# Kernel tuning notes

Measured on AMD Instinct MI355X. Metric: run time of the kernel, lower is better.

## Reference

```python
import jax, jax.numpy as jnp
import numpy as np

# Dimensions
B_, T_, IN_ = 8, 1024, 512          # batch, seq_len, in_dim
D_ = 1024                           # latent_dim (hidden_size)
I_ = 2048                           # intermediate_size
N_ = 64                             # state_size
H_ = 16                             # ssm_num_head
P_ = I_ // H_                       # head_dim = 128
K_ = 3                              # conv_kernel
L_ = 4                              # num_layer
OUT_, CB_ = 512, 1024               # out_dim, num_code_book
CONV_DIM = I_ + 2 * N_              # 2176
PROJ = I_ + CONV_DIM + H_           # in_proj width of mixer = 4240


def setup_inputs() -> dict:
    key = jax.random.key(0)
    ks = jax.random.split(key, 16)
    s = 0.02
    inp = {
        "x": jax.random.normal(ks[0], (B_, T_, IN_), jnp.float32),
        "in_w": jax.random.normal(ks[1], (IN_, D_), jnp.float32) * s,
        "in_b": jnp.zeros((D_,), jnp.float32),
        "norm_w": jnp.ones((L_, D_), jnp.float32),
        "mix_in_w": jax.random.normal(ks[2], (L_, D_, PROJ), jnp.float32) * s,
        "conv_w": jax.random.normal(ks[3], (L_, K_, 1, CONV_DIM), jnp.float32) * s,
        "conv_b": jnp.zeros((L_, CONV_DIM), jnp.float32),
        "dt_bias": jax.random.normal(ks[4], (L_, H_), jnp.float32) * 0.1,
        "A_log": jnp.log(jax.random.uniform(ks[5], (L_, H_), jnp.float32, 0.001, 0.1)),
        "D": jnp.ones((L_, H_), jnp.float32),
        "gnorm_w": jnp.ones((L_, I_), jnp.float32),
        "mix_out_w": jax.random.normal(ks[6], (L_, I_, D_), jnp.float32) * s,
        "out_w": jax.random.normal(ks[7], (D_, OUT_), jnp.float32) * s,
        "out_b": jnp.zeros((OUT_,), jnp.float32),
        "code_w": jax.random.normal(ks[8], (D_, CB_), jnp.float32) * s,
        "code_b": jnp.zeros((CB_,), jnp.float32),
    }
    return inp


def rmsnorm(x, w, eps=1e-6):
    v = jnp.mean(jnp.square(x), axis=-1, keepdims=True)
    return x * jax.lax.rsqrt(v + eps) * w


def mamba_block(x, nw, inw, cw, cb, dtb, alog, Dv, gnw, outw):
    residual = x
    h = rmsnorm(x, nw)
    proj = h @ inw                                   # [B,T,PROJ]
    gate, hBC, dt = jnp.split(proj, [I_, I_ + CONV_DIM], axis=-1)
    # causal depthwise conv along time
    conv = jax.lax.conv_general_dilated(
        hBC, cw, window_strides=(1,), padding=[(K_ - 1, 0)],
        dimension_numbers=("NWC", "WIO", "NWC"), feature_group_count=CONV_DIM)
    conv = jax.nn.silu(conv + cb)
    xs, Bm, Cm = jnp.split(conv, [I_, I_ + N_], axis=-1)   # [B,T,I],[B,T,N],[B,T,N]
    dt = jax.nn.softplus(dt + dtb)                   # [B,T,H]
    a = -jnp.exp(alog)                               # [H] scalar decay per head
    xh = xs.reshape(B_, T_, H_, P_)

    def step(hst, inp):
        dt_t, B_t, C_t, x_t = inp                    # [B,H],[B,N],[B,N],[B,H,P]
        dA = jnp.exp(dt_t * a)                       # [B,H]
        hst = hst * dA[:, :, None, None] + (dt_t[:, :, None, None] * x_t[..., None]) * B_t[:, None, None, :]
        y = jnp.einsum("bhpn,bn->bhp", hst, C_t)
        return hst, y

    inputs = (dt.transpose(1, 0, 2), Bm.transpose(1, 0, 2),
              Cm.transpose(1, 0, 2), xh.transpose(1, 0, 2, 3))
    h0 = jnp.zeros((B_, H_, P_, N_), x.dtype)
    _, ys = jax.lax.scan(step, h0, inputs)           # ys: [T,B,H,P]
    y = ys.transpose(1, 0, 2, 3) + Dv[None, None, :, None] * xh
    y = y.reshape(B_, T_, I_)
    y = rmsnorm(y * jax.nn.silu(gate), gnw)          # gated RMSNorm
    return residual + y @ outw


def reference(x, in_w, in_b, norm_w, mix_in_w, conv_w, conv_b, dt_bias,
              A_log, D, gnorm_w, mix_out_w, out_w, out_b, code_w, code_b):
    h = x @ in_w + in_b
    for i in range(L_):
        h = mamba_block(h, norm_w[i], mix_in_w[i], conv_w[i], conv_b[i],
                        dt_bias[i], A_log[i], D[i], gnorm_w[i], mix_out_w[i])
    return (h @ out_w + out_b, h @ code_w + code_b)
```

## Files before the change

kernel.cpp:

```cpp
#include <hip/hip_runtime.h>
#include <hip/hip_bf16.h>

typedef __hip_bfloat16 bf16;
typedef __bf16 bfv8 __attribute__((ext_vector_type(8)));
typedef float fv4 __attribute__((ext_vector_type(4)));

#define B_  8
#define T_  1024
#define INP 512
#define D_  1024
#define I_  2048
#define N_  64
#define H_  16
#define P_  128
#define L_  4
#define OUT_ 512
#define CB_ 1024
#define CONV_DIM 2176
#define PROJ 4240
#define M_  (B_*T_)
#define TC  64
#define NC  (T_/TC)

typedef const __attribute__((address_space(1))) void gv_t;
typedef __attribute__((address_space(3))) void lv_t;

__device__ __forceinline__ void load_lds16(const bf16* g, char* l) {
    __builtin_amdgcn_global_load_lds((gv_t*)g, (lv_t*)l, 16, 0, 0);
}

template <int N> __device__ __forceinline__ void wait_vm() {
    if constexpr (N == 0) asm volatile("s_waitcnt vmcnt(0)" ::: "memory");
    else if constexpr (N == 6) asm volatile("s_waitcnt vmcnt(6)" ::: "memory");
    else asm volatile("s_waitcnt vmcnt(8)" ::: "memory");
}
__device__ __forceinline__ void barrier_sync() {
    asm volatile("s_barrier" ::: "memory");
}

__global__ __launch_bounds__(256) void ingest_k(const float* __restrict__ src,
                                                bf16* __restrict__ dst, int n) {
    int i = blockIdx.x * 256 + threadIdx.x;
    if (i >= n) return;
    dst[i] = __float2bfloat16(src[i]);
}

__global__ __launch_bounds__(256) void transpose_any(const float* __restrict__ in,
                                                     size_t off,
                                                     bf16* __restrict__ out,
                                                     int R, int C) {
    __shared__ bf16 tile[32][33];
    int c0 = blockIdx.x * 32, r0 = blockIdx.y * 32;
    int tx = threadIdx.x, ty = threadIdx.y;
#pragma unroll
    for (int i = 0; i < 4; ++i) {
        int r = r0 + ty + i * 8, c = c0 + tx;
        bf16 v = __float2bfloat16(0.f);
        if (c < C) v = __float2bfloat16(in[off + (size_t)r * C + c]);
        tile[ty + i * 8][tx] = v;
    }
    __syncthreads();
#pragma unroll
    for (int i = 0; i < 4; ++i) {
        int c = c0 + ty + i * 8;
        out[(size_t)c * R + r0 + tx] = tile[tx][ty + i * 8];
    }
}

template <int MODE, int BN, int WGM, int WGN>
__global__ __launch_bounds__(512) void gemm256(const bf16* __restrict__ A,
                                               const bf16* __restrict__ Bt,
                                               int K, int N,
                                               const bf16* __restrict__ bias,
                                               float* __restrict__ outF,
                                               bf16* __restrict__ outB,
                                               bf16* __restrict__ outB2,
                                               float* __restrict__ outF2) {
    constexpr int BM = 256, BK = 64;
    constexpr int MT = BM / WGM / 16;
    constexpr int NT = BN / WGN / 16;
    constexpr int ABYTES = BM * BK * 2;
    constexpr int BBYTES = BN * BK * 2;
    constexpr int BUF = ABYTES + BBYTES;
    constexpr int AL = ABYTES / 8192;
    constexpr int BL = BBYTES / 8192;
    constexpr int LOADS = AL + BL;

    extern __shared__ char lds[];

    const int tid = threadIdx.x;
    const int wv = tid >> 6, lane = tid & 63;
    const int l16 = lane & 15, quad = lane >> 4;
    const int wm = (wv / WGN) * (BM / WGM);
    const int wn = (wv % WGN) * (BN / WGN);

    const int NX = gridDim.x;
    const int nwg = NX * gridDim.y;
    const int orig = blockIdx.y * NX + blockIdx.x;
    const int q = nwg >> 3, r = nwg & 7, xcd = orig & 7, lid = orig >> 3;
    const int wg = (xcd < r ? xcd * (q + 1) : r * (q + 1) + (xcd - r) * q) + lid;
    const int m0 = (wg / NX) * BM;
    const int n0 = (wg % NX) * BN;

    const int srow = tid >> 3, sslot = tid & 7;
    const int swz = (sslot ^ (srow & 7)) << 3;
    const bf16* ga = A  + (size_t)(m0 + srow) * K + swz;
    const bf16* gb = Bt + (size_t)(n0 + srow) * K + swz;
    char* la0 = lds + wv * 1024;
    char* lb0 = lds + ABYTES + wv * 1024;

    auto stage = [&](int k0, int b) {
#pragma unroll
        for (int j = 0; j < AL; ++j)
            load_lds16(ga + (size_t)(j * 64) * K + k0, la0 + b * BUF + j * 8192);
#pragma unroll
        for (int j = 0; j < BL; ++j)
            load_lds16(gb + (size_t)(j * 64) * K + k0, lb0 + b * BUF + j * 8192);
    };

    const int KT = K / BK;
    stage(0, 0);
    stage(BK, 1);
    wait_vm<LOADS>();
    barrier_sync();

    fv4 acc[MT][NT] = {};

    for (int t = 0; t < KT; ++t) {
        const char* Ab = lds + (t & 1) * BUF;
        const char* Bb = Ab + ABYTES;
#pragma unroll
        for (int kk = 0; kk < 2; ++kk) {
            bfv8 af[MT], bfr[NT];
#pragma unroll
            for (int i = 0; i < MT; ++i) {
                int rr = wm + i * 16 + l16;
                af[i] = *(const bfv8*)(Ab + rr * 128 +
                        ((((kk << 2) + quad) ^ (rr & 7)) << 4));
            }
#pragma unroll
            for (int i = 0; i < NT; ++i) {
                int rr = wn + i * 16 + l16;
                bfr[i] = *(const bfv8*)(Bb + rr * 128 +
                         ((((kk << 2) + quad) ^ (rr & 7)) << 4));
            }
            __builtin_amdgcn_s_setprio(1);
#pragma unroll
            for (int mt = 0; mt < MT; ++mt)
#pragma unroll
                for (int nt = 0; nt < NT; ++nt)
                    acc[mt][nt] = __builtin_amdgcn_mfma_f32_16x16x32_bf16(
                        af[mt], bfr[nt], acc[mt][nt], 0, 0, 0);
            __builtin_amdgcn_s_setprio(0);
        }
        if (t + 1 < KT) {
            asm volatile("s_waitcnt lgkmcnt(0)" ::: "memory");
            barrier_sync();
            if (t + 2 < KT) {
                stage((t + 2) * BK, t & 1);
                wait_vm<LOADS>();
            } else {
                wait_vm<0>();
            }
            barrier_sync();
        }
    }

#pragma unroll
    for (int mt = 0; mt < MT; ++mt) {
#pragma unroll
        for (int nt = 0; nt < NT; ++nt) {
#pragma unroll
            for (int i = 0; i < 4; ++i) {
                int row = m0 + wm + mt * 16 + quad * 4 + i;
                int col = n0 + wn + nt * 16 + l16;
                float v = acc[mt][nt][i];
                if (MODE == 0) {
                    v += __bfloat162float(bias[col]);
                    outF[(size_t)row * N + col] = v;
                } else if (MODE == 1) {
                    if (col < I_)
                        outB[(size_t)row * I_ + col] = __float2bfloat16(v);
                    else if (col < I_ + CONV_DIM)
                        outB2[(size_t)row * CONV_DIM + (col - I_)] = __float2bfloat16(v);
                    else if (col < PROJ)
                        outF2[(size_t)row * H_ + (col - (I_ + CONV_DIM))] = v;
                } else if (MODE == 2) {
                    outF[(size_t)row * N + col] += v;
                }
            }
        }
    }
}

__global__ __launch_bounds__(256) void rmsnorm_k(const float* __restrict__ x,
                                                 const bf16* __restrict__ w,
                                                 bf16* __restrict__ out) {
    int row = blockIdx.x, tid = threadIdx.x;
    float4 v = *(const float4*)&x[(size_t)row * D_ + tid * 4];
    float ss = v.x * v.x + v.y * v.y + v.z * v.z + v.w * v.w;
#pragma unroll
    for (int off = 32; off; off >>= 1) ss += __shfl_down(ss, off);
    __shared__ float sb[4];
    if ((tid & 63) == 0) sb[tid >> 6] = ss;
    __syncthreads();
    ss = sb[0] + sb[1] + sb[2] + sb[3];
    float rs = rsqrtf(ss * (1.f / D_) + 1e-6f);
    float xv[4] = {v.x, v.y, v.z, v.w};
#pragma unroll
    for (int j = 0; j < 4; ++j)
        out[(size_t)row * D_ + tid * 4 + j] =
            __float2bfloat16(xv[j] * rs * __bfloat162float(w[tid * 4 + j]));
}

__global__ __launch_bounds__(256) void gatednorm_k(const bf16* __restrict__ y,
                                                   const bf16* __restrict__ g,
                                                   const bf16* __restrict__ w,
                                                   bf16* __restrict__ out) {
    int row = blockIdx.x, tid = threadIdx.x;
    size_t base = (size_t)row * I_ + tid * 8;
    bf16 yv[8], gv[8];
    *(uint4*)yv = *(const uint4*)&y[base];
    *(uint4*)gv = *(const uint4*)&g[base];
    float vv[8]; float ss = 0.f;
#pragma unroll
    for (int j = 0; j < 8; ++j) {
        float yf = __bfloat162float(yv[j]);
        float gf = __bfloat162float(gv[j]);
        float sig = 1.f / (1.f + expf(-gf));
        vv[j] = yf * gf * sig;
        ss += vv[j] * vv[j];
    }
#pragma unroll
    for (int off = 32; off; off >>= 1) ss += __shfl_down(ss, off);
    __shared__ float sb[4];
    if ((tid & 63) == 0) sb[tid >> 6] = ss;
    __syncthreads();
    ss = sb[0] + sb[1] + sb[2] + sb[3];
    float rs = rsqrtf(ss * (1.f / I_) + 1e-6f);
    bf16 ov[8];
#pragma unroll
    for (int j = 0; j < 8; ++j)
        ov[j] = __float2bfloat16(vv[j] * rs * __bfloat162float(w[tid * 8 + j]));
    *(uint4*)&out[base] = *(uint4*)ov;
}

__global__ __launch_bounds__(256) void conv_k(const bf16* __restrict__ hbc,
                                              const bf16* __restrict__ w,
                                              const bf16* __restrict__ bias,
                                              bf16* __restrict__ xs,
                                              float* __restrict__ bc) {
    int cq = blockIdx.x * 256 + threadIdx.x;
    if (cq >= CONV_DIM / 4) return;
    int c = cq * 4;
    int bt = blockIdx.y;
    int t = bt & (T_ - 1);
    float acc[4];
#pragma unroll
    for (int j = 0; j < 4; ++j) acc[j] = __bfloat162float(bias[c + j]);
#pragma unroll
    for (int k = 0; k < 3; ++k) {
        int tt = t - 2 + k;
        if (tt < 0) continue;
        const bf16* src = &hbc[(size_t)(bt - 2 + k) * CONV_DIM + c];
#pragma unroll
        for (int j = 0; j < 4; ++j)
            acc[j] = fmaf(__bfloat162float(w[k * CONV_DIM + c + j]),
                          __bfloat162float(src[j]), acc[j]);
    }
#pragma unroll
    for (int j = 0; j < 4; ++j) {
        float v = acc[j];
        v = v / (1.f + expf(-v));
        if (c + j < I_) xs[(size_t)bt * I_ + c + j] = __float2bfloat16(v);
        else            bc[(size_t)bt * 128 + (c + j - I_)] = v;
    }
}

__global__ __launch_bounds__(256) void dtprep_k(const float* __restrict__ dtraw,
                                                const float* __restrict__ dtb,
                                                const float* __restrict__ alog,
                                                float* __restrict__ wco,
                                                float* __restrict__ gma) {
    int chain = blockIdx.x * 4 + (threadIdx.x >> 6);
    int s = threadIdx.x & 63;
    int h = chain & 15, ci = (chain >> 4) & (NC - 1), b = chain >> 8;
    float a = -expf(alog[h]);
    float bz = dtb[h];
    int idx = (b * T_ + ci * TC + s) * H_ + h;
    float z = dtraw[idx] + bz;
    float dt = fmaxf(z, 0.f) + log1pf(expf(-fabsf(z)));
    float ps = dt * a;
#pragma unroll
    for (int d = 1; d < 64; d <<= 1) {
        float o = __shfl_up(ps, d, 64);
        if (s >= d) ps += o;
    }
    float g = expf(ps);
    wco[idx] = dt / g;
    gma[idx] = g;
}

__global__ __launch_bounds__(128) void scan_local_k(const bf16* __restrict__ xs,
                                                    const float* __restrict__ bc,
                                                    const float* __restrict__ wco,
                                                    const float* __restrict__ gma,
                                                    const float* __restrict__ dvec,
                                                    bf16* __restrict__ yout,
                                                    bf16* __restrict__ sfin) {
    int bid = blockIdx.x;
    int ci = bid & (NC - 1);
    int h  = (bid >> 4) & (H_ - 1);
    int b  = bid >> 8;
    int p = threadIdx.x;
    float Dv = dvec[h];
    float st[64];
#pragma unroll
    for (int n = 0; n < 64; ++n) st[n] = 0.f;
    int bt0 = b * T_ + ci * TC;
    const bf16* xptr = xs + (size_t)bt0 * I_ + h * P_ + p;
    bf16* yptr = yout + (size_t)bt0 * I_ + h * P_ + p;
    float xv_n = __bfloat162float(xptr[0]);
    for (int s = 0; s < TC; ++s) {
        float xv = xv_n;
        if (s + 1 < TC) xv_n = __bfloat162float(xptr[(size_t)(s + 1) * I_]);
        float w = wco[(bt0 + s) * H_ + h];
        float g = gma[(bt0 + s) * H_ + h];
        float cc = w * xv;
        const float4* B4 = (const float4*)&bc[(size_t)(bt0 + s) * 128];
#pragma unroll
        for (int j = 0; j < 16; ++j) {
            float4 bv = B4[j];
            st[4 * j + 0] = fmaf(cc, bv.x, st[4 * j + 0]);
            st[4 * j + 1] = fmaf(cc, bv.y, st[4 * j + 1]);
            st[4 * j + 2] = fmaf(cc, bv.z, st[4 * j + 2]);
            st[4 * j + 3] = fmaf(cc, bv.w, st[4 * j + 3]);
        }
        float y0 = 0.f, y1 = 0.f, y2 = 0.f, y3 = 0.f;
#pragma unroll
        for (int j = 0; j < 16; ++j) {
            float4 cv = B4[16 + j];
            y0 = fmaf(st[4 * j + 0], cv.x, y0);
            y1 = fmaf(st[4 * j + 1], cv.y, y1);
            y2 = fmaf(st[4 * j + 2], cv.z, y2);
            y3 = fmaf(st[4 * j + 3], cv.w, y3);
        }
        yptr[(size_t)s * I_] = __float2bfloat16(fmaf(g, (y0 + y1) + (y2 + y3), Dv * xv));
    }
    float G = gma[(bt0 + TC - 1) * H_ + h];
    bf16* sf = sfin + (size_t)bid * (128 * 64);
#pragma unroll
    for (int n = 0; n < 64; ++n) sf[n * 128 + p] = __float2bfloat16(st[n] * G);
}

__global__ __launch_bounds__(128) void scan_combine_k(bf16* __restrict__ sbuf,
                                                      const float* __restrict__ gma) {
    int bid = blockIdx.x;
    int n = bid & 63;
    int h = (bid >> 6) & (H_ - 1);
    int b = bid >> 10;
    int p = threadIdx.x;
    size_t base0 = ((size_t)(b * (H_ * NC) + h * NC) * (128 * 64)) + n * 128 + p;
    int gbase = b * T_ * H_ + h;
    float S = 0.f;
#pragma unroll
    for (int ci = 0; ci < NC; ++ci) {
        bf16* addr = sbuf + base0 + (size_t)ci * (128 * 64);
        float tmp = __bfloat162float(*addr);
        *addr = __float2bfloat16(S);
        float G = gma[gbase + (ci * TC + TC - 1) * H_];
        S = fmaf(G, S, tmp);
    }
}

__global__ __launch_bounds__(128) void scan_correct_k(const bf16* __restrict__ sinit,
                                                      const float* __restrict__ gma,
                                                      const float* __restrict__ bc,
                                                      bf16* __restrict__ yout) {
    int bid = blockIdx.x;
    int ci = bid & (NC - 1);
    if (ci == 0) return;
    int h = (bid >> 4) & (H_ - 1);
    int b = bid >> 8;
    int p = threadIdx.x;
    const bf16* sb = sinit + (size_t)bid * (128 * 64);
    float S[64];
#pragma unroll
    for (int n = 0; n < 64; ++n) S[n] = __bfloat162float(sb[n * 128 + p]);
    int bt0 = b * T_ + ci * TC;
    bf16* yptr = yout + (size_t)bt0 * I_ + h * P_ + p;
    for (int s = 0; s < TC; ++s) {
        float g = gma[(bt0 + s) * H_ + h];
        const float4* C4 = (const float4*)&bc[(size_t)(bt0 + s) * 128 + 64];
        float y0 = 0.f, y1 = 0.f, y2 = 0.f, y3 = 0.f;
#pragma unroll
        for (int j = 0; j < 16; ++j) {
            float4 cv = C4[j];
            y0 = fmaf(S[4 * j + 0], cv.x, y0);
            y1 = fmaf(S[4 * j + 1], cv.y, y1);
            y2 = fmaf(S[4 * j + 2], cv.z, y2);
            y3 = fmaf(S[4 * j + 3], cv.w, y3);
        }
        float y = __bfloat162float(yptr[(size_t)s * I_]);
        yptr[(size_t)s * I_] = __float2bfloat16(fmaf(g, (y0 + y1) + (y2 + y3), y));
    }
}

__global__ __launch_bounds__(256) void cast_f2b_k(const float* __restrict__ in,
                                                  bf16* __restrict__ out) {
    int i = (blockIdx.x * 256 + threadIdx.x) * 4;
    float4 v = *(const float4*)&in[i];
    bf16 ov[4] = {__float2bfloat16(v.x), __float2bfloat16(v.y),
                  __float2bfloat16(v.z), __float2bfloat16(v.w)};
    *(uint2*)&out[i] = *(uint2*)ov;
}


static inline size_t align256(size_t x) { return (x + 255) & ~(size_t)255; }

extern "C" void kernel_launch(void* const* d_in, const int* in_sizes, int n_in,
                              void* d_out, int out_size, void* d_ws, size_t ws_size,
                              hipStream_t stream) {
    const float* x_in     = (const float*)d_in[0];
    const float* in_w     = (const float*)d_in[1];
    const float* in_b     = (const float*)d_in[2];
    const float* norm_w   = (const float*)d_in[3];
    const float* mix_in_w = (const float*)d_in[4];
    const float* conv_w   = (const float*)d_in[5];
    const float* conv_b   = (const float*)d_in[6];
    const float* dt_bias  = (const float*)d_in[7];
    const float* A_log    = (const float*)d_in[8];
    const float* Dvec     = (const float*)d_in[9];
    const float* gnorm_w  = (const float*)d_in[10];
    const float* mix_out_w= (const float*)d_in[11];
    const float* out_w    = (const float*)d_in[12];
    const float* out_b    = (const float*)d_in[13];
    const float* code_w   = (const float*)d_in[14];
    const float* code_b   = (const float*)d_in[15];
    float* outF0 = (float*)d_out;
    float* outF1 = (float*)d_out + (size_t)M_ * OUT_;

    char* p = (char*)d_ws;
    auto alloc = [&](size_t bytes) -> char* { char* r = p; p += align256(bytes); return r; };

    bf16*  xb       = (bf16*)alloc((size_t)M_ * INP * 2);
    bf16*  v_inb    = (bf16*)alloc(D_ * 2);
    bf16*  v_normw  = (bf16*)alloc(L_ * D_ * 2);
    bf16*  v_convw  = (bf16*)alloc(L_ * 3 * CONV_DIM * 2);
    bf16*  v_convb  = (bf16*)alloc(L_ * CONV_DIM * 2);
    bf16*  v_gnw    = (bf16*)alloc(L_ * I_ * 2);
    bf16*  v_outb   = (bf16*)alloc(OUT_ * 2);
    bf16*  v_codeb  = (bf16*)alloc(CB_ * 2);
    bf16*  wt_in    = (bf16*)alloc((size_t)1024 * 512 * 2);
    bf16*  wt_big   = (bf16*)alloc((size_t)4352 * 1024 * 2);
    bf16*  wt_small = (bf16*)alloc((size_t)1024 * 2048 * 2);
    bf16*  wt_out   = (bf16*)alloc((size_t)512 * 1024 * 2);
    bf16*  wt_code  = (bf16*)alloc((size_t)1024 * 1024 * 2);
    float* hbuf     = (float*)alloc((size_t)M_ * D_ * 4);
    bf16*  hn       = (bf16*)alloc((size_t)M_ * D_ * 2);
    bf16*  gate     = (bf16*)alloc((size_t)M_ * I_ * 2);
    bf16*  hbc      = (bf16*)alloc((size_t)M_ * CONV_DIM * 2);
    float* dtraw    = (float*)alloc((size_t)M_ * H_ * 4);
    bf16*  xs       = (bf16*)alloc((size_t)M_ * I_ * 2);
    float* bcbuf    = (float*)alloc((size_t)M_ * 128 * 4);
    float* wcob     = (float*)alloc((size_t)M_ * H_ * 4);
    float* gmab     = (float*)alloc((size_t)M_ * H_ * 4);
    bf16*  sfin     = (bf16*)alloc((size_t)B_ * H_ * NC * 128 * 64 * 2);
    (void)in_sizes; (void)n_in; (void)out_size;

    size_t needed = (size_t)(p - (char*)d_ws);
    if (needed > ws_size) return;

    constexpr size_t SH256 = 131072;
    constexpr size_t SH128 = 98304;
    static bool attr_done = false;
    if (!attr_done) {
        attr_done = true;
        (void)hipFuncSetAttribute((const void*)gemm256<0, 128, 4, 2>,
                                  hipFuncAttributeMaxDynamicSharedMemorySize, (int)SH256);
        (void)hipFuncSetAttribute((const void*)gemm256<1, 256, 2, 4>,
                                  hipFuncAttributeMaxDynamicSharedMemorySize, (int)SH256);
        (void)hipFuncSetAttribute((const void*)gemm256<2, 128, 4, 2>,
                                  hipFuncAttributeMaxDynamicSharedMemorySize, (int)SH256);
    }

    auto ing = [&](const float* src, bf16* dst, int n) {
        ingest_k<<<(n + 255) / 256, 256, 0, stream>>>(src, dst, n);
    };
    ing(x_in, xb, M_ * INP);
    ing(in_b, v_inb, D_);
    ing(norm_w, v_normw, L_ * D_);
    ing(conv_w, v_convw, L_ * 3 * CONV_DIM);
    ing(conv_b, v_convb, L_ * CONV_DIM);
    ing(gnorm_w, v_gnw, L_ * I_);
    ing(out_b, v_outb, OUT_);
    ing(code_b, v_codeb, CB_);

    dim3 tb(32, 8);
    transpose_any<<<dim3(32, 16), tb, 0, stream>>>(in_w, 0, wt_in, 512, 1024);
    transpose_any<<<dim3(16, 32), tb, 0, stream>>>(out_w, 0, wt_out, 1024, 512);
    transpose_any<<<dim3(32, 32), tb, 0, stream>>>(code_w, 0, wt_code, 1024, 1024);

    gemm256<0, 128, 4, 2><<<dim3(8, 32), 512, SH128, stream>>>(
        xb, wt_in, INP, D_, v_inb, hbuf, nullptr, nullptr, nullptr);

    for (int i = 0; i < L_; ++i) {
        transpose_any<<<dim3(136, 32), tb, 0, stream>>>(mix_in_w, (size_t)i * 1024 * PROJ,
                                                        wt_big, 1024, PROJ);
        transpose_any<<<dim3(32, 64), tb, 0, stream>>>(mix_out_w, (size_t)i * 2048 * 1024,
                                                       wt_small, 2048, 1024);
        rmsnorm_k<<<M_, 256, 0, stream>>>(hbuf, v_normw + i * D_, hn);
        gemm256<1, 256, 2, 4><<<dim3(17, 32), 512, SH256, stream>>>(
            hn, wt_big, D_, 4352, nullptr, nullptr, gate, hbc, dtraw);
        conv_k<<<dim3(3, M_), 256, 0, stream>>>(hbc, v_convw + i * 3 * CONV_DIM,
                                                v_convb + i * CONV_DIM, xs, bcbuf);
        dtprep_k<<<B_ * NC * H_ / 4, 256, 0, stream>>>(
            dtraw, dt_bias + i * H_, A_log + i * H_, wcob, gmab);
        scan_local_k<<<B_ * H_ * NC, 128, 0, stream>>>(xs, bcbuf, wcob, gmab,
                                                       Dvec + i * H_, hbc, sfin);
        scan_combine_k<<<B_ * H_ * 64, 128, 0, stream>>>(sfin, gmab);
        scan_correct_k<<<B_ * H_ * NC, 128, 0, stream>>>(sfin, gmab, bcbuf, hbc);
        gatednorm_k<<<M_, 256, 0, stream>>>(hbc, gate, v_gnw + i * I_, xs);
        gemm256<2, 128, 4, 2><<<dim3(8, 32), 512, SH128, stream>>>(
            xs, wt_small, I_, D_, nullptr, hbuf, nullptr, nullptr, nullptr);
    }

    cast_f2b_k<<<(M_ * D_) / 1024, 256, 0, stream>>>(hbuf, hn);
    gemm256<0, 128, 4, 2><<<dim3(4, 32), 512, SH128, stream>>>(
        hn, wt_out, D_, OUT_, v_outb, outF0, nullptr, nullptr, nullptr);
    gemm256<0, 128, 4, 2><<<dim3(8, 32), 512, SH128, stream>>>(
        hn, wt_code, D_, CB_, v_codeb, outF1, nullptr, nullptr, nullptr);
}
```

Measured before the change: 1.957 ms.

## Rewrite GEMM main loop as multi-stage ring pipeline with half-K tiles

Replaces the double-buffered BK=64 GEMM loop with a ring of 3 or 4 stages at K=32 per stage. Loads for the next stage are issued between the LDS fragment reads and the MFMAs, and each iteration has one barrier instead of two. For the wide in-projection GEMM the compute is split into two M halves so the B-tile load can go in between them. The aim is deeper prefetch and less barrier stall, at the cost of more loop iterations, a changed LDS swizzle and a smaller LDS footprint for the BN=128 variants.

```diff
diff --git a/kernel.cpp b/kernel.cpp
--- a/kernel.cpp
+++ b/kernel.cpp
@@ -31,7 +31,8 @@
 
 template <int N> __device__ __forceinline__ void wait_vm() {
     if constexpr (N == 0) asm volatile("s_waitcnt vmcnt(0)" ::: "memory");
-    else if constexpr (N == 6) asm volatile("s_waitcnt vmcnt(6)" ::: "memory");
+    else if constexpr (N == 3) asm volatile("s_waitcnt vmcnt(3)" ::: "memory");
+    else if constexpr (N == 4) asm volatile("s_waitcnt vmcnt(4)" ::: "memory");
     else asm volatile("s_waitcnt vmcnt(8)" ::: "memory");
 }
 __device__ __forceinline__ void barrier_sync() {
@@ -67,27 +68,28 @@
     }
 }
 
-template <int MODE, int BN, int WGM, int WGN>
-__global__ __launch_bounds__(512) void gemm256(const bf16* __restrict__ A,
-                                               const bf16* __restrict__ Bt,
-                                               int K, int N,
-                                               const bf16* __restrict__ bias,
-                                               float* __restrict__ outF,
-                                               bf16* __restrict__ outB,
-                                               bf16* __restrict__ outB2,
-                                               float* __restrict__ outF2) {
-    constexpr int BM = 256, BK = 64;
+template <int MODE, int BN, int WGM, int WGN, int RING>
+__global__ __launch_bounds__(512) void gemm8p(const bf16* __restrict__ A,
+                                              const bf16* __restrict__ Bt,
+                                              int K, int N,
+                                              const bf16* __restrict__ bias,
+                                              float* __restrict__ outF,
+                                              bf16* __restrict__ outB,
+                                              bf16* __restrict__ outB2,
+                                              float* __restrict__ outF2) {
+    constexpr int BM = 256, HK = 32;
     constexpr int MT = BM / WGM / 16;
     constexpr int NT = BN / WGN / 16;
-    constexpr int ABYTES = BM * BK * 2;
-    constexpr int BBYTES = BN * BK * 2;
-    constexpr int BUF = ABYTES + BBYTES;
-    constexpr int AL = ABYTES / 8192;
-    constexpr int BL = BBYTES / 8192;
-    constexpr int LOADS = AL + BL;
+    constexpr int SUB = (BN == 256) ? 2 : 1;
+    constexpr int MTS = MT / SUB;
+    constexpr int ABY = BM * HK * 2;
+    constexpr int BBY = BN * HK * 2;
+    constexpr int BUF = ABY + BBY;
+    constexpr int AL = ABY / 8192;
+    constexpr int BL = BBY / 8192;
+    constexpr int LD = AL + BL;
 
     extern __shared__ char lds[];
-
     const int tid = threadIdx.x;
     const int wv = tid >> 6, lane = tid & 63;
     const int l16 = lane & 15, quad = lane >> 4;
@@ -102,68 +104,92 @@
     const int m0 = (wg / NX) * BM;
     const int n0 = (wg % NX) * BN;
 
-    const int srow = tid >> 3, sslot = tid & 7;
-    const int swz = (sslot ^ (srow & 7)) << 3;
+    const int srow = tid >> 2, sslot = tid & 3;
+    const int swz = (sslot ^ ((srow >> 1) & 3)) << 3;
     const bf16* ga = A  + (size_t)(m0 + srow) * K + swz;
     const bf16* gb = Bt + (size_t)(n0 + srow) * K + swz;
-    char* la0 = lds + wv * 1024;
-    char* lb0 = lds + ABYTES + wv * 1024;
-
-    auto stage = [&](int k0, int b) {
+    char* lw = lds + wv * 1024;
+
+    const int HT = K / HK;
+
+    auto stageA = [&](int stg, int rbuf) {
 #pragma unroll
         for (int j = 0; j < AL; ++j)
-            load_lds16(ga + (size_t)(j * 64) * K + k0, la0 + b * BUF + j * 8192);
+            load_lds16(ga + (size_t)stg * HK + (size_t)(j * 128) * K,
+                       lw + rbuf * BUF + j * 8192);
+    };
+    auto stageB = [&](int stg, int rbuf) {
 #pragma unroll
         for (int j = 0; j < BL; ++j)
-            load_lds16(gb + (size_t)(j * 64) * K + k0, lb0 + b * BUF + j * 8192);
+            load_lds16(gb + (size_t)stg * HK + (size_t)(j * 128) * K,
+                       lw + rbuf * BUF + ABY + j * 8192);
     };
 
-    const int KT = K / BK;
-    stage(0, 0);
-    stage(BK, 1);
-    wait_vm<LOADS>();
+#pragma unroll
+    for (int h = 0; h < RING - 1; ++h) { stageA(h, h); stageB(h, h); }
+    if constexpr (RING == 4) wait_vm<8>(); else wait_vm<3>();
     barrier_sync();
 
     fv4 acc[MT][NT] = {};
-
-    for (int t = 0; t < KT; ++t) {
-        const char* Ab = lds + (t & 1) * BUF;
-        const char* Bb = Ab + ABYTES;
-#pragma unroll
-        for (int kk = 0; kk < 2; ++kk) {
-            bfv8 af[MT], bfr[NT];
-#pragma unroll
-            for (int i = 0; i < MT; ++i) {
-                int rr = wm + i * 16 + l16;
-                af[i] = *(const bfv8*)(Ab + rr * 128 +
-                        ((((kk << 2) + quad) ^ (rr & 7)) << 4));
+    int rb = 0;
+    for (int ht = 0; ht < HT; ++ht) {
+        const char* Ab = lds + rb * BUF;
+        const char* Bb = Ab + ABY;
+        const int stg = ht + RING - 1;
+        const int sb = (rb == 0) ? RING - 1 : rb - 1;
+        const bool dostage = stg < HT;
+
+        bfv8 bf[NT], af[MTS];
+#pragma unroll
+        for (int i = 0; i < NT; ++i) {
+            int rr = wn + i * 16 + l16;
+            bf[i] = *(const bfv8*)(Bb + rr * 64 + ((quad ^ ((rr >> 1) & 3)) << 4));
+        }
+#pragma unroll
+        for (int i = 0; i < MTS; ++i) {
+            int rr = wm + i * 16 + l16;
+            af[i] = *(const bfv8*)(Ab + rr * 64 + ((quad ^ ((rr >> 1) & 3)) << 4));
+        }
+        if (dostage) stageA(stg, sb);
+        if constexpr (SUB == 1) { if (dostage) stageB(stg, sb); }
+        __builtin_amdgcn_s_setprio(1);
+#pragma unroll
+        for (int mt = 0; mt < MTS; ++mt)
+#pragma unroll
+            for (int nt = 0; nt < NT; ++nt)
+                acc[mt][nt] = __builtin_amdgcn_mfma_f32_16x16x32_bf16(
+                    af[mt], bf[nt], acc[mt][nt], 0, 0, 0);
+        __builtin_amdgcn_s_setprio(0);
+
+        if constexpr (SUB == 2) {
+            barrier_sync();
+            bfv8 af2[MTS];
+#pragma unroll
+            for (int i = 0; i < MTS; ++i) {
+                int rr = wm + (MTS + i) * 16 + l16;
+                af2[i] = *(const bfv8*)(Ab + rr * 64 + ((quad ^ ((rr >> 1) & 3)) << 4));
             }
-#pragma unroll
-            for (int i = 0; i < NT; ++i) {
-                int rr = wn + i * 16 + l16;
-                bfr[i] = *(const bfv8*)(Bb + rr * 128 +
-                         ((((kk << 2) + quad) ^ (rr & 7)) << 4));
-            }
+            if (dostage) stageB(stg, sb);
             __builtin_amdgcn_s_setprio(1);
 #pragma unroll
-            for (int mt = 0; mt < MT; ++mt)
+            for (int mt = 0; mt < MTS; ++mt)
 #pragma unroll
                 for (int nt = 0; nt < NT; ++nt)
-                    acc[mt][nt] = __builtin_amdgcn_mfma_f32_16x16x32_bf16(
-                        af[mt], bfr[nt], acc[mt][nt], 0, 0, 0);
+                    acc[MTS + mt][nt] = __builtin_amdgcn_mfma_f32_16x16x32_bf16(
+                        af2[mt], bf[nt], acc[MTS + mt][nt], 0, 0, 0);
             __builtin_amdgcn_s_setprio(0);
         }
-        if (t + 1 < KT) {
-            asm volatile("s_waitcnt lgkmcnt(0)" ::: "memory");
-            barrier_sync();
-            if (t + 2 < KT) {
-                stage((t + 2) * BK, t & 1);
-                wait_vm<LOADS>();
-            } else {
-                wait_vm<0>();
-            }
-            barrier_sync();
-        }
+
+        int fut = HT - 1 - ht; if (fut > RING - 1) fut = RING - 1;
+        if (fut >= 1) {
+            int w = (fut - 1) * LD;
+            if (w >= 8) wait_vm<8>();
+            else if (w == 4) wait_vm<4>();
+            else if (w == 3) wait_vm<3>();
+            else wait_vm<0>();
+        }
+        barrier_sync();
+        rb = (rb + 1 == RING) ? 0 : rb + 1;
     }
 
 #pragma unroll
@@ -472,16 +498,16 @@
     if (needed > ws_size) return;
 
     constexpr size_t SH256 = 131072;
-    constexpr size_t SH128 = 98304;
+    constexpr size_t SH128 = 73728;
     static bool attr_done = false;
     if (!attr_done) {
         attr_done = true;
-        (void)hipFuncSetAttribute((const void*)gemm256<0, 128, 4, 2>,
+        (void)hipFuncSetAttribute((const void*)gemm8p<1, 256, 2, 4, 4>,
                                   hipFuncAttributeMaxDynamicSharedMemorySize, (int)SH256);
-        (void)hipFuncSetAttribute((const void*)gemm256<1, 256, 2, 4>,
-                                  hipFuncAttributeMaxDynamicSharedMemorySize, (int)SH256);
-        (void)hipFuncSetAttribute((const void*)gemm256<2, 128, 4, 2>,
-                                  hipFuncAttributeMaxDynamicSharedMemorySize, (int)SH256);
+        (void)hipFuncSetAttribute((const void*)gemm8p<0, 128, 4, 2, 3>,
+                                  hipFuncAttributeMaxDynamicSharedMemorySize, (int)SH128);
+        (void)hipFuncSetAttribute((const void*)gemm8p<2, 128, 4, 2, 3>,
+                                  hipFuncAttributeMaxDynamicSharedMemorySize, (int)SH128);
     }
 
     auto ing = [&](const float* src, bf16* dst, int n) {
@@ -501,7 +527,7 @@
     transpose_any<<<dim3(16, 32), tb, 0, stream>>>(out_w, 0, wt_out, 1024, 512);
     transpose_any<<<dim3(32, 32), tb, 0, stream>>>(code_w, 0, wt_code, 1024, 1024);
 
-    gemm256<0, 128, 4, 2><<<dim3(8, 32), 512, SH128, stream>>>(
+    gemm8p<0, 128, 4, 2, 3><<<dim3(8, 32), 512, SH128, stream>>>(
         xb, wt_in, INP, D_, v_inb, hbuf, nullptr, nullptr, nullptr);
 
     for (int i = 0; i < L_; ++i) {
@@ -510,7 +536,7 @@
         transpose_any<<<dim3(32, 64), tb, 0, stream>>>(mix_out_w, (size_t)i * 2048 * 1024,
                                                        wt_small, 2048, 1024);
         rmsnorm_k<<<M_, 256, 0, stream>>>(hbuf, v_normw + i * D_, hn);
-        gemm256<1, 256, 2, 4><<<dim3(17, 32), 512, SH256, stream>>>(
+        gemm8p<1, 256, 2, 4, 4><<<dim3(17, 32), 512, SH256, stream>>>(
             hn, wt_big, D_, 4352, nullptr, nullptr, gate, hbc, dtraw);
         conv_k<<<dim3(3, M_), 256, 0, stream>>>(hbc, v_convw + i * 3 * CONV_DIM,
                                                 v_convb + i * CONV_DIM, xs, bcbuf);
@@ -521,13 +547,13 @@
         scan_combine_k<<<B_ * H_ * 64, 128, 0, stream>>>(sfin, gmab);
         scan_correct_k<<<B_ * H_ * NC, 128, 0, stream>>>(sfin, gmab, bcbuf, hbc);
         gatednorm_k<<<M_, 256, 0, stream>>>(hbc, gate, v_gnw + i * I_, xs);
-        gemm256<2, 128, 4, 2><<<dim3(8, 32), 512, SH128, stream>>>(
+        gemm8p<2, 128, 4, 2, 3><<<dim3(8, 32), 512, SH128, stream>>>(
             xs, wt_small, I_, D_, nullptr, hbuf, nullptr, nullptr, nullptr);
     }
 
     cast_f2b_k<<<(M_ * D_) / 1024, 256, 0, stream>>>(hbuf, hn);
-    gemm256<0, 128, 4, 2><<<dim3(4, 32), 512, SH128, stream>>>(
+    gemm8p<0, 128, 4, 2, 3><<<dim3(4, 32), 512, SH128, stream>>>(
         hn, wt_out, D_, OUT_, v_outb, outF0, nullptr, nullptr, nullptr);
-    gemm256<0, 128, 4, 2><<<dim3(8, 32), 512, SH128, stream>>>(
+    gemm8p<0, 128, 4, 2, 3><<<dim3(8, 32), 512, SH128, stream>>>(
         hn, wt_code, D_, CB_, v_codeb, outF1, nullptr, nullptr, nullptr);
 }
```

Result: no change. 1.932 ms (-1.3%).
